# Kernel tuning notes

Hardware: AMD Instinct MI355X
Metric: run time of the kernel (lower is better)

## Reference

```python
import jax, jax.numpy as jnp
from jax import lax
import numpy as np

B = 4096        # num_batch
NVAR = 120      # 3 * num_legs(4) * horizon(10)
NC = 2 * NVAR   # num_constraints = 240
HID = 1024      # GRU hidden size
RIN = 3 * (NC + NVAR)  # GRU input dim = 1080
MAXITER = 8
RHO = 1.0
REG = 1e-4


def setup_inputs() -> dict:
    key = jax.random.key(0)
    ks = jax.random.split(key, 10)
    # SPD quadratic cost H, linear cost g, inequality constraints C x <= c
    M = jax.random.normal(ks[0], (NVAR, NVAR), jnp.float32)
    H = M @ M.T / NVAR + jnp.eye(NVAR, dtype=jnp.float32)
    g = jax.random.normal(ks[1], (NVAR,), jnp.float32)
    C = 0.1 * jax.random.normal(ks[2], (NC, NVAR), jnp.float32)
    c = jax.random.uniform(ks[3], (NC,), jnp.float32, 0.1, 1.0)
    lamda_init = jax.random.normal(ks[4], (B, NVAR), jnp.float32)
    s_init = jax.random.uniform(ks[5], (B, NC), jnp.float32)
    h_0 = jnp.zeros((B, HID), jnp.float32)
    # GRU cell (torch GRUCell layout: [3*HID, in]) + output head to NC+NVAR
    sc_i = 1.0 / np.sqrt(RIN)
    sc_h = 1.0 / np.sqrt(HID)
    W_ih = sc_i * jax.random.normal(ks[6], (3 * HID, RIN), jnp.float32)
    b_ih = jnp.zeros((3 * HID,), jnp.float32)
    W_hh = sc_h * jax.random.normal(ks[7], (3 * HID, HID), jnp.float32)
    b_hh = jnp.zeros((3 * HID,), jnp.float32)
    W_out = sc_h * jax.random.normal(ks[8], (NC + NVAR, HID), jnp.float32)
    b_out = jnp.zeros((NC + NVAR,), jnp.float32)
    return dict(lamda_init=lamda_init, s_init=s_init, h_0=h_0, H=H, g=g, C=C, c=c,
                W_ih=W_ih, b_ih=b_ih, W_hh=W_hh, b_hh=b_hh, W_out=W_out, b_out=b_out)


def _gru_cell(x, h, W_ih, b_ih, W_hh, b_hh):
    gi = x @ W_ih.T + b_ih
    gh = h @ W_hh.T + b_hh
    i_r, i_z, i_n = jnp.split(gi, 3, axis=1)
    h_r, h_z, h_n = jnp.split(gh, 3, axis=1)
    r = jax.nn.sigmoid(i_r + h_r)
    z = jax.nn.sigmoid(i_z + h_z)
    n = jnp.tanh(i_n + r * h_n)
    return (1.0 - z) * n + z * h


def reference(lamda_init, s_init, h_0, H, g, C, c, W_ih, b_ih, W_hh, b_hh, W_out, b_out):
    I = jnp.eye(NVAR, dtype=H.dtype)
    # ---- init solve (compute_projection_gru preamble) ----
    Q_inv0 = jnp.linalg.pinv(H + REG * I)
    lincost0 = -0.0 * lamda_init + g                 # [B, NVAR]
    xi0 = (-lincost0) @ Q_inv0.T                     # sol = (Qinv @ rhs.T).T
    s0 = jnp.maximum(0.0, -(xi0 @ C.T) + c)
    s0 = 0.0 * s_init + s0                           # s_init = 0*nn + 1*s_
    lam0 = lamda_init
    # ---- constant per-iteration projection matrix (same every iter) ----
    Q_inv = jnp.linalg.pinv(H + RHO * (C.T @ C) + REG * I)

    def step(carry, _):
        s, lam, h = carry
        # compute_feasible_control
        b_aug = c - s                                # [B, NC]
        lincost = -lam + g - RHO * (b_aug @ C)       # [B, NVAR]
        xi = (-lincost) @ Q_inv.T                    # [B, NVAR]
        Axi = xi @ C.T                               # [B, NC]
        s_new = jnp.maximum(0.0, -Axi + c)
        res_vec = Axi - c + s_new
        res_norm = jnp.linalg.norm(res_vec, axis=1)
        lam_new = lam - RHO * (res_vec @ C)
        qp_cost = 0.5 * (xi @ H @ xi.T) + xi @ g     # [B, B] (faithful to source)
        qp_norm = jnp.linalg.norm(qp_cost, axis=1)
        # GRU refinement
        r = jnp.concatenate([s, lam, s_new, lam_new, s_new - s, lam_new - lam], axis=1)
        h_new = _gru_cell(r, h, W_ih, b_ih, W_hh, b_hh)
        out = h_new @ W_out.T + b_out                # [B, NC+NVAR]
        s_fin = jnp.maximum(0.0, s_new + out[:, :NC])
        lam_fin = lam_new + out[:, NC:NC + NVAR]
        fixed = jnp.linalg.norm(lam - lam_fin, axis=1) + jnp.linalg.norm(s - s_fin, axis=1)
        return (s_fin, lam_fin, h_new), (xi, res_norm, fixed, qp_norm)

    (_, _, _), (xis, primal, fixed, qpres) = lax.scan(step, (s0, lam0, h_0), None, length=MAXITER)
    return xis[-1], primal, fixed, qpres
```

## Files before the change

### kernel.cpp

```cpp
#include <hip/hip_runtime.h>
#include <hip/hip_bf16.h>
#include <math.h>

#define NB    4096
#define NV    120
#define NCN   240
#define HIDD  1024
#define RINN  1080
#define NOUTD 360
#define NOUTP 384
#define NITER 8
#define REGEPS 1e-4f
#define NPART 128

#define KCAT 4224
#define HOFF 2176
#define KWC  2112
#define KWO  1024
#define NSTEP_R 34
#define NSTEPS  66

typedef unsigned short u16;
typedef __attribute__((ext_vector_type(8))) short short8v;
typedef __attribute__((ext_vector_type(4))) float f32x4;

__device__ inline u16 f2b(float x) {
    __hip_bfloat16 h = __float2bfloat16(x);
    return __builtin_bit_cast(u16, h);
}
__device__ inline float b2f(u16 u) {
    __hip_bfloat16 h = __builtin_bit_cast(__hip_bfloat16, u);
    return __bfloat162float(h);
}

__device__ inline void gl16(const void* g, void* l) {
    __builtin_amdgcn_global_load_lds(
        (__attribute__((address_space(1))) void*)(void*)g,
        (__attribute__((address_space(3))) void*)l, 16, 0, 0);
}

__global__ void k_buildA(const float* __restrict__ H, const float* __restrict__ C,
                         float* __restrict__ A, float* __restrict__ A0) {
    int i = blockIdx.x;
    int which = blockIdx.y;
    for (int j = threadIdx.x; j < NV; j += blockDim.x) {
        float v = H[i*NV + j] + (i == j ? REGEPS : 0.f);
        if (which == 0) {
            float acc = 0.f;
            for (int k = 0; k < NCN; ++k) acc += C[k*NV + i] * C[k*NV + j];
            A[i*NV + j] = v + acc;
        } else {
            A0[i*NV + j] = v;
        }
    }
}

__device__ inline void inv4x4(const float* m, float* inv) {
    float s0 = m[0]*m[5] - m[1]*m[4];
    float s1 = m[0]*m[6] - m[2]*m[4];
    float s2 = m[0]*m[7] - m[3]*m[4];
    float s3 = m[1]*m[6] - m[2]*m[5];
    float s4 = m[1]*m[7] - m[3]*m[5];
    float s5 = m[2]*m[7] - m[3]*m[6];
    float c5 = m[10]*m[15] - m[11]*m[14];
    float c4 = m[9]*m[15] - m[11]*m[13];
    float c3 = m[9]*m[14] - m[10]*m[13];
    float c2 = m[8]*m[15] - m[11]*m[12];
    float c1 = m[8]*m[14] - m[10]*m[12];
    float c0 = m[8]*m[13] - m[9]*m[12];
    float det = s0*c5 - s1*c4 + s2*c3 + s3*c2 - s4*c1 + s5*c0;
    float id = 1.0f / det;
    inv[0]  = ( m[5]*c5 - m[6]*c4 + m[7]*c3) * id;
    inv[1]  = (-m[1]*c5 + m[2]*c4 - m[3]*c3) * id;
    inv[2]  = ( m[13]*s5 - m[14]*s4 + m[15]*s3) * id;
    inv[3]  = (-m[9]*s5 + m[10]*s4 - m[11]*s3) * id;
    inv[4]  = (-m[4]*c5 + m[6]*c2 - m[7]*c1) * id;
    inv[5]  = ( m[0]*c5 - m[2]*c2 + m[3]*c1) * id;
    inv[6]  = (-m[12]*s5 + m[14]*s2 - m[15]*s1) * id;
    inv[7]  = ( m[8]*s5 - m[10]*s2 + m[11]*s1) * id;
    inv[8]  = ( m[4]*c4 - m[5]*c2 + m[7]*c0) * id;
    inv[9]  = (-m[0]*c4 + m[1]*c2 - m[3]*c0) * id;
    inv[10] = ( m[12]*s4 - m[13]*s2 + m[15]*s0) * id;
    inv[11] = (-m[8]*s4 + m[9]*s2 - m[11]*s0) * id;
    inv[12] = (-m[4]*c3 + m[5]*c1 - m[6]*c0) * id;
    inv[13] = ( m[0]*c3 - m[1]*c1 + m[2]*c0) * id;
    inv[14] = (-m[12]*s3 + m[13]*s1 - m[14]*s0) * id;
    inv[15] = ( m[8]*s3 - m[9]*s1 + m[10]*s0) * id;
}

__global__ __launch_bounds__(1024) void k_invert(const float* __restrict__ Ain,
                                                 const float* __restrict__ A0in,
                                                 float* __restrict__ Qi,
                                                 float* __restrict__ Qi0) {
    __shared__ float M[NV][132];
    __shared__ float Rl[4][132];
    __shared__ float Bl[16];
    const float* src = (blockIdx.x == 0) ? Ain : A0in;
    float* dst = (blockIdx.x == 0) ? Qi : Qi0;
    const int t = threadIdx.x;
    for (int idx = t; idx < NV*132; idx += 1024) {
        int i = idx / 132, j = idx - i*132;
        M[i][j] = (j < NV) ? src[i*NV + j] : 0.f;
    }
    __syncthreads();
    const int ty = t >> 5;
    const int g4 = (t & 31) * 4;
    for (int kk = 0; kk < NV; kk += 4) {
        if (ty == 0) {
            float a[16], b[16];
            #pragma unroll
            for (int p = 0; p < 4; ++p) {
                float4 v = *(const float4*)&M[kk + p][kk];
                a[p*4+0] = v.x; a[p*4+1] = v.y; a[p*4+2] = v.z; a[p*4+3] = v.w;
            }
            inv4x4(a, b);
            float4 m0v = *(const float4*)&M[kk+0][g4];
            float4 m1v = *(const float4*)&M[kk+1][g4];
            float4 m2v = *(const float4*)&M[kk+2][g4];
            float4 m3v = *(const float4*)&M[kk+3][g4];
            #pragma unroll
            for (int p = 0; p < 4; ++p) {
                float4 r;
                r.x = b[p*4+0]*m0v.x + b[p*4+1]*m1v.x + b[p*4+2]*m2v.x + b[p*4+3]*m3v.x;
                r.y = b[p*4+0]*m0v.y + b[p*4+1]*m1v.y + b[p*4+2]*m2v.y + b[p*4+3]*m3v.y;
                r.z = b[p*4+0]*m0v.z + b[p*4+1]*m1v.z + b[p*4+2]*m2v.z + b[p*4+3]*m3v.z;
                r.w = b[p*4+0]*m0v.w + b[p*4+1]*m1v.w + b[p*4+2]*m2v.w + b[p*4+3]*m3v.w;
                *(float4*)&Rl[p][g4] = r;
            }
            if (t < 16) Bl[t] = b[t];
        }
        float4 F[4];
        #pragma unroll
        for (int q = 0; q < 4; ++q) {
            int i = ty + 32*q;
            F[q] = (i < NV) ? *(const float4*)&M[i][kk] : float4{0.f,0.f,0.f,0.f};
        }
        __syncthreads();
        #pragma unroll
        for (int q = 0; q < 4; ++q) {
            int i = ty + 32*q;
            if (i < NV) {
                int dp = i - kk;
                bool ispiv = (dp >= 0) && (dp < 4);
                float4 v;
                if (g4 == kk) {
                    if (ispiv) {
                        v = *(const float4*)&Bl[dp*4];
                    } else {
                        v.x = -(F[q].x*Bl[0] + F[q].y*Bl[4] + F[q].z*Bl[8]  + F[q].w*Bl[12]);
                        v.y = -(F[q].x*Bl[1] + F[q].y*Bl[5] + F[q].z*Bl[9]  + F[q].w*Bl[13]);
                        v.z = -(F[q].x*Bl[2] + F[q].y*Bl[6] + F[q].z*Bl[10] + F[q].w*Bl[14]);
                        v.w = -(F[q].x*Bl[3] + F[q].y*Bl[7] + F[q].z*Bl[11] + F[q].w*Bl[15]);
                    }
                } else if (ispiv) {
                    v = *(const float4*)&Rl[dp][g4];
                } else {
                    float4 r0 = *(const float4*)&Rl[0][g4];
                    float4 r1 = *(const float4*)&Rl[1][g4];
                    float4 r2 = *(const float4*)&Rl[2][g4];
                    float4 r3 = *(const float4*)&Rl[3][g4];
                    v = *(const float4*)&M[i][g4];
                    v.x -= F[q].x*r0.x + F[q].y*r1.x + F[q].z*r2.x + F[q].w*r3.x;
                    v.y -= F[q].x*r0.y + F[q].y*r1.y + F[q].z*r2.y + F[q].w*r3.y;
                    v.z -= F[q].x*r0.z + F[q].y*r1.z + F[q].z*r2.z + F[q].w*r3.z;
                    v.w -= F[q].x*r0.w + F[q].y*r1.w + F[q].z*r2.w + F[q].w*r3.w;
                }
                *(float4*)&M[i][g4] = v;
            }
        }
        __syncthreads();
    }
    for (int idx = t; idx < NV*NV; idx += 1024) {
        int i = idx / NV, j = idx - i*NV;
        dst[idx] = M[i][j];
    }
}

__global__ void k_s0(const float* __restrict__ Qi0, const float* __restrict__ g,
                     const float* __restrict__ C, const float* __restrict__ c,
                     float* __restrict__ s0v) {
    __shared__ float xi0[NV];
    int t = threadIdx.x;
    if (t < NV) {
        float a = 0.f;
        for (int j = 0; j < NV; ++j) a += Qi0[t*NV + j] * g[j];
        xi0[t] = -a;
    }
    __syncthreads();
    if (t < NCN) {
        float a = 0.f;
        for (int j = 0; j < NV; ++j) a += C[t*NV + j] * xi0[j];
        s0v[t] = fmaxf(0.f, c[t] - a);
    }
}

__global__ void k_init(const float* __restrict__ s0v, const float* __restrict__ lam0,
                       float* __restrict__ s, float* __restrict__ lam) {
    int b0 = blockIdx.x * 8;
    int t = threadIdx.x;
    for (int idx = t; idx < 8*NCN; idx += 256) {
        int m = idx / NCN, k = idx % NCN;
        s[(size_t)(b0 + m)*NCN + k] = s0v[k];
    }
    for (int idx = t; idx < 8*NV; idx += 256) lam[(size_t)b0*NV + idx] = lam0[(size_t)b0*NV + idx];
}

__global__ void k_packH(const float* __restrict__ h0, u16* __restrict__ act) {
    int n = blockIdx.x;
    size_t base = (size_t)n * KCAT + HOFF;
    for (int k = threadIdx.x; k < HIDD; k += 256) {
        float x = h0[(size_t)n * HIDD + k];
        u16 hi = f2b(x);
        act[base + k] = hi;
        act[base + HIDD + k] = f2b(x - b2f(hi));
    }
}

__global__ void k_packWcat(const float* __restrict__ Wih, const float* __restrict__ Whh,
                           u16* __restrict__ Wc) {
    int n = blockIdx.x;
    size_t base = (size_t)n * KWC;
    for (int k = threadIdx.x; k < 1088; k += 256)
        Wc[base + k] = f2b(k < RINN ? Wih[(size_t)n * RINN + k] : 0.f);
    for (int k = threadIdx.x; k < HIDD; k += 256)
        Wc[base + 1088 + k] = f2b(Whh[(size_t)n * HIDD + k]);
}

__global__ void k_packWo(const float* __restrict__ src, u16* __restrict__ dst) {
    int n = blockIdx.x;
    size_t row = (size_t)n * KWO;
    for (int k = threadIdx.x; k < KWO; k += 256)
        dst[row + k] = f2b(n < NOUTD ? src[(size_t)n * HIDD + k] : 0.f);
}

__device__ inline void write2(u16* __restrict__ act, size_t base, int pos, float x) {
    u16 hi = f2b(x);
    u16 lo = f2b(x - b2f(hi));
    act[base + pos] = hi;
    act[base + 1088 + pos] = lo;
}

#define XB 8
__global__ __launch_bounds__(512) void k_xiproj(
        const float* __restrict__ s, const float* __restrict__ lam,
        const float* __restrict__ Cg, const float* __restrict__ c,
        const float* __restrict__ g, const float* __restrict__ Qi,
        const float* __restrict__ Hg,
        float* __restrict__ xi, float* __restrict__ Y, float* __restrict__ wv,
        float* __restrict__ snew, float* __restrict__ lamn,
        u16* __restrict__ act, float* __restrict__ primal) {
    __shared__ float Msh[NCN][125];
    __shared__ float bd[XB][NCN];
    __shared__ float ul[XB][NV];
    __shared__ float xl[XB][NV];
    __shared__ float resl[XB][NCN];
    const int b0 = blockIdx.x * XB;
    const int t = threadIdx.x;

    for (int idx = t; idx < XB*NCN; idx += 512) {
        int m = idx / NCN, k = idx % NCN;
        bd[m][k] = c[k] - s[(size_t)(b0 + m)*NCN + k];
    }
    for (int idx = t; idx < NCN*NV; idx += 512) {
        int i = idx / NV, j = idx - i*NV;
        Msh[i][j] = Cg[idx];
    }
    __syncthreads();
    for (int idx = t; idx < XB*NV; idx += 512) {
        int m = idx / NV, j = idx - m*NV;
        float a0 = 0.f, a1 = 0.f, a2 = 0.f, a3 = 0.f;
        for (int k = 0; k < NCN; k += 4) {
            a0 += bd[m][k]     * Msh[k][j];
            a1 += bd[m][k + 1] * Msh[k + 1][j];
            a2 += bd[m][k + 2] * Msh[k + 2][j];
            a3 += bd[m][k + 3] * Msh[k + 3][j];
        }
        ul[m][j] = lam[(size_t)(b0 + m)*NV + j] - g[j] + ((a0 + a1) + (a2 + a3));
    }
    __syncthreads();
    for (int idx = t; idx < NV*NV; idx += 512) {
        int i = idx / NV, j = idx - i*NV;
        Msh[i][j] = Qi[idx];
        Msh[120 + i][j] = Hg[idx];
    }
    __syncthreads();
    for (int idx = t; idx < XB*NV; idx += 512) {
        int m = idx / NV, i = idx - m*NV;
        float a0 = 0.f, a1 = 0.f, a2 = 0.f, a3 = 0.f;
        for (int j = 0; j < NV; j += 4) {
            a0 += Msh[j][i]     * ul[m][j];
            a1 += Msh[j + 1][i] * ul[m][j + 1];
            a2 += Msh[j + 2][i] * ul[m][j + 2];
            a3 += Msh[j + 3][i] * ul[m][j + 3];
        }
        float a = (a0 + a1) + (a2 + a3);
        xl[m][i] = a;
        xi[(size_t)(b0 + m)*NV + i] = a;
    }
    __syncthreads();
    for (int idx = t; idx < XB*NV; idx += 512) {
        int m = idx / NV, i = idx - m*NV;
        float a0 = 0.f, a1 = 0.f, a2 = 0.f, a3 = 0.f;
        for (int j = 0; j < NV; j += 4) {
            a0 += xl[m][j]     * Msh[120 + j][i];
            a1 += xl[m][j + 1] * Msh[121 + j][i];
            a2 += xl[m][j + 2] * Msh[122 + j][i];
            a3 += xl[m][j + 3] * Msh[123 + j][i];
        }
        Y[(size_t)(b0 + m)*NV + i] = (a0 + a1) + (a2 + a3);
    }
    if (t < XB) {
        float a = 0.f;
        for (int j = 0; j < NV; ++j) a += xl[t][j] * g[j];
        wv[b0 + t] = a;
    }
    __syncthreads();
    for (int idx = t; idx < NCN*NV; idx += 512) {
        int i = idx / NV, j = idx - i*NV;
        Msh[i][j] = Cg[idx];
    }
    __syncthreads();
    for (int idx = t; idx < XB*NCN; idx += 512) {
        int m = idx / NCN, k = idx - m*NCN;
        float a0 = 0.f, a1 = 0.f, a2 = 0.f, a3 = 0.f;
        for (int j = 0; j < NV; j += 4) {
            a0 += Msh[k][j]     * xl[m][j];
            a1 += Msh[k][j + 1] * xl[m][j + 1];
            a2 += Msh[k][j + 2] * xl[m][j + 2];
            a3 += Msh[k][j + 3] * xl[m][j + 3];
        }
        float a = (a0 + a1) + (a2 + a3);
        float sn = fmaxf(0.f, c[k] - a);
        float rv = a - c[k] + sn;
        resl[m][k] = rv;
        int b = b0 + m;
        snew[(size_t)b*NCN + k] = sn;
        float so = s[(size_t)b*NCN + k];
        size_t base = (size_t)b * KCAT;
        write2(act, base, k, so);
        write2(act, base, 360 + k, sn);
        write2(act, base, 720 + k, sn - so);
    }
    __syncthreads();
    if (t < XB) {
        float a = 0.f;
        for (int k = 0; k < NCN; ++k) a += resl[t][k] * resl[t][k];
        primal[b0 + t] = sqrtf(a);
    }
    for (int idx = t; idx < XB*NV; idx += 512) {
        int m = idx / NV, i = idx - m*NV;
        float a0 = 0.f, a1 = 0.f, a2 = 0.f, a3 = 0.f;
        for (int k = 0; k < NCN; k += 4) {
            a0 += resl[m][k]     * Msh[k][i];
            a1 += resl[m][k + 1] * Msh[k + 1][i];
            a2 += resl[m][k + 2] * Msh[k + 2][i];
            a3 += resl[m][k + 3] * Msh[k + 3][i];
        }
        float a = (a0 + a1) + (a2 + a3);
        int b = b0 + m;
        float lo = lam[(size_t)b*NV + i];
        float ln = lo - a;
        lamn[(size_t)b*NV + i] = ln;
        size_t base = (size_t)b * KCAT;
        write2(act, base, 240 + i, lo);
        write2(act, base, 600 + i, ln);
        write2(act, base, 960 + i, ln - lo);
    }
    for (int idx = t; idx < XB*8; idx += 512) {
        int m = idx >> 3, k = 1080 + (idx & 7);
        size_t base = (size_t)(b0 + m) * KCAT;
        act[base + k] = 0;
        act[base + 1088 + k] = 0;
    }
}

__global__ __launch_bounds__(256) void k_qp_part(const float* __restrict__ xi, const float* __restrict__ wv,
                         double* __restrict__ Gp, double* __restrict__ vp, double* __restrict__ Sp) {
    __shared__ float xl[32][NV];
    __shared__ float wl[32];
    int p = blockIdx.x;
    int b0 = p * 32;
    int t = threadIdx.x;
    for (int idx = t; idx < 32*NV; idx += 256) xl[idx/NV][idx%NV] = xi[(size_t)b0*NV + idx];
    if (t < 32) wl[t] = wv[b0 + t];
    __syncthreads();
    for (int idx = t; idx < NV*NV; idx += 256) {
        int i = idx / NV, j = idx % NV;
        double a = 0.0;
        for (int m = 0; m < 32; ++m) a += (double)xl[m][i] * (double)xl[m][j];
        Gp[(size_t)p*NV*NV + idx] = a;
    }
    if (t < NV) {
        double a = 0.0;
        for (int m = 0; m < 32; ++m) a += (double)wl[m] * (double)xl[m][t];
        vp[(size_t)p*NV + t] = a;
    }
    if (t == 0) {
        double a = 0.0;
        for (int m = 0; m < 32; ++m) a += (double)wl[m] * (double)wl[m];
        Sp[p] = a;
    }
}

__global__ void k_qp_red(const double* __restrict__ Gp, const double* __restrict__ vp,
                         const double* __restrict__ Sp,
                         double* __restrict__ G, double* __restrict__ v, double* __restrict__ S) {
    int idx = blockIdx.x * 256 + threadIdx.x;
    if (idx < NV*NV) {
        double a = 0.0;
        for (int p = 0; p < NPART; ++p) a += Gp[(size_t)p*NV*NV + idx];
        G[idx] = a;
    }
    if (idx < NV) {
        double a = 0.0;
        for (int p = 0; p < NPART; ++p) a += vp[(size_t)p*NV + idx];
        v[idx] = a;
    }
    if (idx == 0) {
        double a = 0.0;
        for (int p = 0; p < NPART; ++p) a += Sp[p];
        S[0] = a;
    }
}

__global__ __launch_bounds__(256) void k_qp_norm(const float* __restrict__ Y, const double* __restrict__ G,
                         const double* __restrict__ v, const double* __restrict__ S,
                         float* __restrict__ qp) {
    __shared__ float Yl[16][NV];
    __shared__ double tl[16][NV];
    int b0 = blockIdx.x * 16;
    int t = threadIdx.x;
    for (int idx = t; idx < 16*NV; idx += 256) Yl[idx/NV][idx%NV] = Y[(size_t)b0*NV + idx];
    __syncthreads();
    for (int idx = t; idx < 16*NV; idx += 256) {
        int m = idx / NV, i = idx % NV;
        double a = 0.0;
        for (int j = 0; j < NV; ++j) a += G[j*NV + i] * (double)Yl[m][j];
        tl[m][i] = a;
    }
    __syncthreads();
    if (t < 16) {
        double a = 0.0, bv = 0.0;
        for (int i = 0; i < NV; ++i) { a += (double)Yl[t][i] * tl[t][i]; bv += (double)Yl[t][i] * v[i]; }
        double q = 0.25 * a + bv + S[0];
        qp[b0 + t] = (float)sqrt(q > 0.0 ? q : 0.0);
    }
}

#define GRUF_STEP(NSLOT, BUFI) do {                                              \
    char* Ah_ = lds + (BUFI) * 40960;                                            \
    char* Al_ = Ah_ + 8192;                                                      \
    char* Bb_ = Ah_ + 16384;                                                     \
    const int srow = lane & 15;                                                  \
    const int ksl = lane >> 4;                                                   \
    short8v ah[2], al[2];                                                        \
    _Pragma("unroll")                                                            \
    for (int fm = 0; fm < 2; ++fm) {                                             \
        int rr = wm * 32 + fm * 16 + srow;                                       \
        int off = rr * 64 + ((ksl ^ ((rr >> 1) & 3)) << 4);                      \
        ah[fm] = *(const short8v*)(Ah_ + off);                                   \
        al[fm] = *(const short8v*)(Al_ + off);                                   \
    }                                                                            \
    __builtin_amdgcn_s_setprio(1);                                               \
    _Pragma("unroll")                                                            \
    for (int fn = 0; fn < 2; ++fn) {                                             \
        int rb = wn * 32 + fn * 16 + srow;                                       \
        int boff = rb * 64 + ((ksl ^ ((rb >> 1) & 3)) << 4);                     \
        short8v bfr = *(const short8v*)(Bb_ + boff);                             \
        short8v bfz = *(const short8v*)(Bb_ + 8192 + boff);                      \
        short8v bfn = *(const short8v*)(Bb_ + 16384 + boff);                     \
        _Pragma("unroll")                                                        \
        for (int fm = 0; fm < 2; ++fm) {                                         \
            acc[0][fn][fm] = __builtin_amdgcn_mfma_f32_16x16x32_bf16(ah[fm], bfr, acc[0][fn][fm], 0, 0, 0); \
            acc[0][fn][fm] = __builtin_amdgcn_mfma_f32_16x16x32_bf16(al[fm], bfr, acc[0][fn][fm], 0, 0, 0); \
            acc[1][fn][fm] = __builtin_amdgcn_mfma_f32_16x16x32_bf16(ah[fm], bfz, acc[1][fn][fm], 0, 0, 0); \
            acc[1][fn][fm] = __builtin_amdgcn_mfma_f32_16x16x32_bf16(al[fm], bfz, acc[1][fn][fm], 0, 0, 0); \
            acc[NSLOT][fn][fm] = __builtin_amdgcn_mfma_f32_16x16x32_bf16(ah[fm], bfn, acc[NSLOT][fn][fm], 0, 0, 0); \
            acc[NSLOT][fn][fm] = __builtin_amdgcn_mfma_f32_16x16x32_bf16(al[fm], bfn, acc[NSLOT][fn][fm], 0, 0, 0); \
        }                                                                        \
    }                                                                            \
    __builtin_amdgcn_s_setprio(0);                                               \
} while (0)

#define GRUF_SYNCN do {                                                          \
    if (wid < 8) { asm volatile("s_waitcnt vmcnt(3)" ::: "memory"); }            \
    else         { asm volatile("s_waitcnt vmcnt(2)" ::: "memory"); }            \
    __builtin_amdgcn_s_barrier();                                                \
    __builtin_amdgcn_sched_barrier(0);                                           \
} while (0)
#define GRUF_SYNC0 do {                                                          \
    asm volatile("s_waitcnt vmcnt(0)" ::: "memory");                             \
    __builtin_amdgcn_s_barrier();                                                \
    __builtin_amdgcn_sched_barrier(0);                                           \
} while (0)

__global__ __launch_bounds__(1024) void k_gruf(
        const u16* __restrict__ act,
        const u16* __restrict__ Wc,
        const float* __restrict__ bih, const float* __restrict__ bhh,
        u16* __restrict__ actn) {
    __shared__ char lds[122880];
    const int t = threadIdx.x;
    const int lane = t & 63;
    const int wid = t >> 6;
    const int wm = wid >> 2;
    const int wn = wid & 3;
    const int bid = blockIdx.x;
    const int xcd = bid & 7;
    const int slot = bid >> 3;
    const int m0 = (xcd * 4 + (slot & 3)) * 128;
    const int n0 = (slot >> 2) * 128;

    f32x4 acc[4][2][2];
    #pragma unroll
    for (int i = 0; i < 4; ++i)
        #pragma unroll
        for (int j = 0; j < 2; ++j)
            #pragma unroll
            for (int k = 0; k < 2; ++k) {
                f32x4 z = {0.f, 0.f, 0.f, 0.f};
                acc[i][j][k] = z;
            }

    auto stage = [&](int step) {
        char* Ah_ = lds + (step % 3) * 40960;
        char* Al_ = Ah_ + 8192;
        char* Bb_ = Ah_ + 16384;
        const int hiOff = (step < NSTEP_R) ? step * 32 : step * 32 + 1088;
        const int loOff = hiOff + ((step < NSTEP_R) ? 1088 : 1024);
        const int wOff = step * 32;
        if (wid >= 8) {
            int q = wid - 8;
            int rr = q * 16 + (lane >> 2);
            int kq = ((lane & 3) ^ ((rr >> 1) & 3)) << 3;
            gl16(act + (size_t)(m0 + rr) * KCAT + hiOff + kq, Ah_ + q * 1024);
            gl16(act + (size_t)(m0 + rr) * KCAT + loOff + kq, Al_ + q * 1024);
        } else {
            #pragma unroll
            for (int j = 0; j < 3; ++j) {
                int cb = wid * 3 + j;
                int rbg = cb * 16 + (lane >> 2);
                int kq = ((lane & 3) ^ ((rbg >> 1) & 3)) << 3;
                gl16(Wc + (size_t)((rbg >> 7) * 1024 + n0 + (rbg & 127)) * KWC + wOff + kq,
                     Bb_ + cb * 1024);
            }
        }
    };

    stage(0);
    stage(1);
    GRUF_SYNCN;
    for (int step = 0; step < NSTEP_R; ++step) {
        stage(step + 2);
        GRUF_STEP(2, step % 3);
        GRUF_SYNCN;
    }
    for (int step = NSTEP_R; step < NSTEPS; ++step) {
        if (step + 2 < NSTEPS) {
            stage(step + 2);
            GRUF_STEP(3, step % 3);
            GRUF_SYNCN;
        } else {
            GRUF_STEP(3, step % 3);
            GRUF_SYNC0;
        }
    }

    #pragma unroll
    for (int fn = 0; fn < 2; ++fn) {
        const int jj = n0 + wn * 32 + fn * 16 + (lane & 15);
        const float bir = bih[jj],        bhr = bhh[jj];
        const float biz = bih[1024 + jj], bhz = bhh[1024 + jj];
        const float bin = bih[2048 + jj], bhn = bhh[2048 + jj];
        #pragma unroll
        for (int fm = 0; fm < 2; ++fm) {
            #pragma unroll
            for (int rg = 0; rg < 4; ++rg) {
                int m = m0 + wm * 32 + fm * 16 + (lane >> 4) * 4 + rg;
                float rz = acc[0][fn][fm][rg];
                float zz = acc[1][fn][fm][rg];
                float inn = acc[2][fn][fm][rg];
                float hnn = acc[3][fn][fm][rg];
                float rgate = 1.f / (1.f + expf(-(rz + bir + bhr)));
                float zgate = 1.f / (1.f + expf(-(zz + biz + bhz)));
                float ngate = tanhf(inn + bin + rgate * (hnn + bhn));
                size_t base = (size_t)m * KCAT + HOFF;
                float hv = b2f(act[base + jj]) + b2f(act[base + HIDD + jj]);
                float hnew = (1.f - zgate) * ngate + zgate * hv;
                u16 nh = f2b(hnew);
                actn[base + jj] = nh;
                actn[base + HIDD + jj] = f2b(hnew - b2f(nh));
            }
        }
    }
}

__global__ __launch_bounds__(512, 2) void k_outp(
        const u16* __restrict__ act, const u16* __restrict__ Wo,
        const float* __restrict__ bo, float* __restrict__ outb) {
    __shared__ char lds[49152];
    const int t = threadIdx.x;
    const int lane = t & 63;
    const int wid = t >> 6;
    const int wm = wid >> 2;
    const int wn = wid & 3;
    const int m0 = blockIdx.x * 128;
    const int n0 = blockIdx.y * 128;
    f32x4 acc[2][4];
    #pragma unroll
    for (int i = 0; i < 2; ++i)
        #pragma unroll
        for (int j = 0; j < 4; ++j) {
            f32x4 z = {0.f, 0.f, 0.f, 0.f};
            acc[i][j] = z;
        }

    auto stage = [&](int step, int buf) {
        char* Ah_ = lds + buf * 24576;
        char* Al_ = Ah_ + 8192;
        char* Bb_ = Ah_ + 16384;
        const int hiOff = HOFF + step * 32;
        const int loOff = HOFF + HIDD + step * 32;
        int s = (wid << 6) + lane;
        int rr = s >> 2;
        int kq = ((lane & 3) ^ ((rr >> 1) & 3)) << 3;
        gl16(act + (size_t)(m0 + rr) * KCAT + hiOff + kq, Ah_ + wid * 1024);
        gl16(act + (size_t)(m0 + rr) * KCAT + loOff + kq, Al_ + wid * 1024);
        gl16(Wo + (size_t)(n0 + rr) * KWO + step * 32 + kq, Bb_ + wid * 1024);
    };

    stage(0, 0);
    __syncthreads();
    int cur = 0;
    for (int step = 0; step < 32; ++step) {
        if (step + 1 < 32) stage(step + 1, cur ^ 1);
        {
            char* Ah_ = lds + cur * 24576;
            char* Al_ = Ah_ + 8192;
            char* Bb_ = Ah_ + 16384;
            const int srow = lane & 15;
            const int ksl = lane >> 4;
            short8v ah[4], al[4];
            #pragma unroll
            for (int fm = 0; fm < 4; ++fm) {
                int rr = wm * 64 + fm * 16 + srow;
                int off = rr * 64 + ((ksl ^ ((rr >> 1) & 3)) << 4);
                ah[fm] = *(const short8v*)(Ah_ + off);
                al[fm] = *(const short8v*)(Al_ + off);
            }
            #pragma unroll
            for (int fn = 0; fn < 2; ++fn) {
                int rb = wn * 32 + fn * 16 + srow;
                int boff = rb * 64 + ((ksl ^ ((rb >> 1) & 3)) << 4);
                short8v bf = *(const short8v*)(Bb_ + boff);
                #pragma unroll
                for (int fm = 0; fm < 4; ++fm) {
                    acc[fn][fm] = __builtin_amdgcn_mfma_f32_16x16x32_bf16(ah[fm], bf, acc[fn][fm], 0, 0, 0);
                    acc[fn][fm] = __builtin_amdgcn_mfma_f32_16x16x32_bf16(al[fm], bf, acc[fn][fm], 0, 0, 0);
                }
            }
        }
        __syncthreads();
        cur ^= 1;
    }
    #pragma unroll
    for (int fn = 0; fn < 2; ++fn) {
        int n = n0 + wn * 32 + fn * 16 + (lane & 15);
        if (n < NOUTD) {
            float bb = bo[n];
            #pragma unroll
            for (int fm = 0; fm < 4; ++fm) {
                #pragma unroll
                for (int rg = 0; rg < 4; ++rg) {
                    int m = m0 + wm * 64 + fm * 16 + (lane >> 4) * 4 + rg;
                    outb[(size_t)m * NOUTP + n] = acc[fn][fm][rg] + bb;
                }
            }
        }
    }
}

__global__ __launch_bounds__(256) void k_fin(const float* __restrict__ snew, const float* __restrict__ lamn,
                     const float* __restrict__ outb,
                     float* __restrict__ s, float* __restrict__ lam,
                     float* __restrict__ fx) {
    __shared__ float redS[16][17];
    __shared__ float redL[16][17];
    int b0 = blockIdx.x * 16;
    int tm = threadIdx.x / 16;
    int tk = threadIdx.x % 16;
    int b = b0 + tm;
    float ds2 = 0.f, dl2 = 0.f;
    for (int k = tk; k < NCN; k += 16) {
        float o = outb[(size_t)b*NOUTP + k];
        float sf = fmaxf(0.f, snew[(size_t)b*NCN + k] + o);
        float so = s[(size_t)b*NCN + k];
        s[(size_t)b*NCN + k] = sf;
        float d = so - sf;
        ds2 += d * d;
    }
    for (int i = tk; i < NV; i += 16) {
        float o = outb[(size_t)b*NOUTP + NCN + i];
        float lf = lamn[(size_t)b*NV + i] + o;
        float lo = lam[(size_t)b*NV + i];
        lam[(size_t)b*NV + i] = lf;
        float d = lo - lf;
        dl2 += d * d;
    }
    redS[tm][tk] = ds2;
    redL[tm][tk] = dl2;
    __syncthreads();
    if (tk == 0) {
        float a = 0.f, l = 0.f;
        for (int q = 0; q < 16; ++q) { a += redS[tm][q]; l += redL[tm][q]; }
        fx[b] = sqrtf(l) + sqrtf(a);
    }
}

extern "C" void kernel_launch(void* const* d_in, const int* in_sizes, int n_in,
                              void* d_out, int out_size, void* d_ws, size_t ws_size,
                              hipStream_t stream) {
    const float* lamda_init = (const float*)d_in[0];
    const float* h0    = (const float*)d_in[2];
    const float* H     = (const float*)d_in[3];
    const float* g     = (const float*)d_in[4];
    const float* C     = (const float*)d_in[5];
    const float* c     = (const float*)d_in[6];
    const float* W_ih  = (const float*)d_in[7];
    const float* b_ih  = (const float*)d_in[8];
    const float* W_hh  = (const float*)d_in[9];
    const float* b_hh  = (const float*)d_in[10];
    const float* W_out = (const float*)d_in[11];
    const float* b_out = (const float*)d_in[12];

    float* out    = (float*)d_out;
    float* xi_out = out;
    float* primal = out + (size_t)NB*NV;
    float* fixedo = primal + (size_t)NITER*NB;
    float* qpres  = fixedo + (size_t)NITER*NB;

    char* wp = (char*)d_ws;
    auto alloc = [&](size_t bytes) {
        void* p = (void*)wp;
        wp += (bytes + 255) & ~(size_t)255;
        return p;
    };
    float* Amat  = (float*)alloc(NV*NV*4);
    float* A0m   = (float*)alloc(NV*NV*4);
    float* Qinv  = (float*)alloc(NV*NV*4);
    float* Qinv0 = (float*)alloc(NV*NV*4);
    float* s0v   = (float*)alloc(NCN*4);
    float* sbuf  = (float*)alloc((size_t)NB*NCN*4);
    float* snew  = (float*)alloc((size_t)NB*NCN*4);
    float* lam   = (float*)alloc((size_t)NB*NV*4);
    float* lamn  = (float*)alloc((size_t)NB*NV*4);
    float* xib   = (float*)alloc((size_t)NB*NV*4);
    float* Yb    = (float*)alloc((size_t)NB*NV*4);
    float* wb    = (float*)alloc(NB*4);
    float* outb  = (float*)alloc((size_t)NB*NOUTP*4);
    u16* actA    = (u16*)alloc((size_t)NB*KCAT*2);
    u16* actB    = (u16*)alloc((size_t)NB*KCAT*2);
    u16* Wcat    = (u16*)alloc((size_t)3072*KWC*2);
    u16* Wopk    = (u16*)alloc((size_t)NOUTP*KWO*2);
    double* Gpart = (double*)alloc((size_t)NPART*NV*NV*8);
    double* vpart = (double*)alloc((size_t)NPART*NV*8);
    double* Spart = (double*)alloc(NPART*8);
    double* Gfin  = (double*)alloc(NV*NV*8);
    double* vfin  = (double*)alloc(NV*8);
    double* Sfin  = (double*)alloc(8);

    k_buildA<<<dim3(NV, 2), dim3(128), 0, stream>>>(H, C, Amat, A0m);
    k_invert<<<dim3(2), dim3(1024), 0, stream>>>(Amat, A0m, Qinv, Qinv0);
    k_s0<<<dim3(1), dim3(256), 0, stream>>>(Qinv0, g, C, c, s0v);
    k_init<<<dim3(NB/8), dim3(256), 0, stream>>>(s0v, lamda_init, sbuf, lam);
    k_packWcat<<<dim3(3072), dim3(256), 0, stream>>>(W_ih, W_hh, Wcat);
    k_packWo<<<dim3(NOUTP), dim3(256), 0, stream>>>(W_out, Wopk);
    k_packH<<<dim3(NB), dim3(256), 0, stream>>>(h0, actA);

    u16* hc = actA;
    u16* hn2 = actB;
    for (int it = 0; it < NITER; ++it) {
        k_xiproj<<<dim3(NB/XB), dim3(512), 0, stream>>>(sbuf, lam, C, c, g, Qinv, H,
                                                        xib, Yb, wb, snew, lamn, hc,
                                                        primal + (size_t)it*NB);
        k_qp_part<<<dim3(NPART), dim3(256), 0, stream>>>(xib, wb, Gpart, vpart, Spart);
        k_qp_red<<<dim3((NV*NV + 255)/256), dim3(256), 0, stream>>>(Gpart, vpart, Spart, Gfin, vfin, Sfin);
        k_qp_norm<<<dim3(NB/16), dim3(256), 0, stream>>>(Yb, Gfin, vfin, Sfin, qpres + (size_t)it*NB);
        k_gruf<<<dim3(256), dim3(1024), 0, stream>>>(hc, Wcat, b_ih, b_hh, hn2);
        k_outp<<<dim3(NB/128, 3), dim3(512), 0, stream>>>(hn2, Wopk, b_out, outb);
        k_fin<<<dim3(NB/16), dim3(256), 0, stream>>>(snew, lamn, outb, sbuf, lam, fixedo + (size_t)it*NB);
        u16* tmp = hc; hc = hn2; hn2 = tmp;
    }
    hipMemcpyAsync(xi_out, xib, (size_t)NB*NV*sizeof(float), hipMemcpyDeviceToDevice, stream);
}
```

Measured before the change: 2.438 ms.

## Shrink GRU and output GEMM tiles, use double buffering, and split QP partials finer

The fused GRU GEMM drops from 128x128 tiles on 1024-thread blocks with a three-stage asynchronous pipeline to 64x128 tiles on 512-thread blocks with plain double buffering and __syncthreads. The setprio hints and the fine-grained vmcnt waits are removed. The output projection moves to 64-row tiles, which doubles its grid, and the QP Gram partials use 16 rows per block across 256 partitions. The goal is more blocks for occupancy and load balance across CUs, at the cost of less weight reuse per tile, more global traffic, and a shallower prefetch pipeline.

```diff
diff --git a/kernel.cpp b/kernel.cpp
--- a/kernel.cpp
+++ b/kernel.cpp
@@ -11,7 +11,7 @@
 #define NOUTP 384
 #define NITER 8
 #define REGEPS 1e-4f
-#define NPART 128
+#define NPART 256
 
 #define KCAT 4224
 #define HOFF 2176
@@ -376,28 +376,28 @@
 
 __global__ __launch_bounds__(256) void k_qp_part(const float* __restrict__ xi, const float* __restrict__ wv,
                          double* __restrict__ Gp, double* __restrict__ vp, double* __restrict__ Sp) {
-    __shared__ float xl[32][NV];
-    __shared__ float wl[32];
+    __shared__ float xl[16][NV];
+    __shared__ float wl[16];
     int p = blockIdx.x;
-    int b0 = p * 32;
+    int b0 = p * 16;
     int t = threadIdx.x;
-    for (int idx = t; idx < 32*NV; idx += 256) xl[idx/NV][idx%NV] = xi[(size_t)b0*NV + idx];
-    if (t < 32) wl[t] = wv[b0 + t];
+    for (int idx = t; idx < 16*NV; idx += 256) xl[idx/NV][idx%NV] = xi[(size_t)b0*NV + idx];
+    if (t < 16) wl[t] = wv[b0 + t];
     __syncthreads();
     for (int idx = t; idx < NV*NV; idx += 256) {
         int i = idx / NV, j = idx % NV;
         double a = 0.0;
-        for (int m = 0; m < 32; ++m) a += (double)xl[m][i] * (double)xl[m][j];
+        for (int m = 0; m < 16; ++m) a += (double)xl[m][i] * (double)xl[m][j];
         Gp[(size_t)p*NV*NV + idx] = a;
     }
     if (t < NV) {
         double a = 0.0;
-        for (int m = 0; m < 32; ++m) a += (double)wl[m] * (double)xl[m][t];
+        for (int m = 0; m < 16; ++m) a += (double)wl[m] * (double)xl[m][t];
         vp[(size_t)p*NV + t] = a;
     }
     if (t == 0) {
         double a = 0.0;
-        for (int m = 0; m < 32; ++m) a += (double)wl[m] * (double)wl[m];
+        for (int m = 0; m < 16; ++m) a += (double)wl[m] * (double)wl[m];
         Sp[p] = a;
     }
 }
@@ -448,9 +448,9 @@
 }
 
 #define GRUF_STEP(NSLOT, BUFI) do {                                              \
-    char* Ah_ = lds + (BUFI) * 40960;                                            \
-    char* Al_ = Ah_ + 8192;                                                      \
-    char* Bb_ = Ah_ + 16384;                                                     \
+    char* Ah_ = lds + (BUFI) * 32768;                                            \
+    char* Al_ = Ah_ + 4096;                                                      \
+    char* Bb_ = Ah_ + 8192;                                                      \
     const int srow = lane & 15;                                                  \
     const int ksl = lane >> 4;                                                   \
     short8v ah[2], al[2];                                                        \
@@ -461,7 +461,6 @@
         ah[fm] = *(const short8v*)(Ah_ + off);                                   \
         al[fm] = *(const short8v*)(Al_ + off);                                   \
     }                                                                            \
-    __builtin_amdgcn_s_setprio(1);                                               \
     _Pragma("unroll")                                                            \
     for (int fn = 0; fn < 2; ++fn) {                                             \
         int rb = wn * 32 + fn * 16 + srow;                                       \
@@ -479,27 +478,14 @@
             acc[NSLOT][fn][fm] = __builtin_amdgcn_mfma_f32_16x16x32_bf16(al[fm], bfn, acc[NSLOT][fn][fm], 0, 0, 0); \
         }                                                                        \
     }                                                                            \
-    __builtin_amdgcn_s_setprio(0);                                               \
 } while (0)
 
-#define GRUF_SYNCN do {                                                          \
-    if (wid < 8) { asm volatile("s_waitcnt vmcnt(3)" ::: "memory"); }            \
-    else         { asm volatile("s_waitcnt vmcnt(2)" ::: "memory"); }            \
-    __builtin_amdgcn_s_barrier();                                                \
-    __builtin_amdgcn_sched_barrier(0);                                           \
-} while (0)
-#define GRUF_SYNC0 do {                                                          \
-    asm volatile("s_waitcnt vmcnt(0)" ::: "memory");                             \
-    __builtin_amdgcn_s_barrier();                                                \
-    __builtin_amdgcn_sched_barrier(0);                                           \
-} while (0)
-
-__global__ __launch_bounds__(1024) void k_gruf(
+__global__ __launch_bounds__(512) void k_gruf(
         const u16* __restrict__ act,
         const u16* __restrict__ Wc,
         const float* __restrict__ bih, const float* __restrict__ bhh,
         u16* __restrict__ actn) {
-    __shared__ char lds[122880];
+    __shared__ char lds[65536];
     const int t = threadIdx.x;
     const int lane = t & 63;
     const int wid = t >> 6;
@@ -508,8 +494,8 @@
     const int bid = blockIdx.x;
     const int xcd = bid & 7;
     const int slot = bid >> 3;
-    const int m0 = (xcd * 4 + (slot & 3)) * 128;
-    const int n0 = (slot >> 2) * 128;
+    const int m0 = (xcd * 8 + (slot & 7)) * 64;
+    const int n0 = (slot >> 3) * 128;
 
     f32x4 acc[4][2][2];
     #pragma unroll
@@ -522,48 +508,45 @@
                 acc[i][j][k] = z;
             }
 
-    auto stage = [&](int step) {
-        char* Ah_ = lds + (step % 3) * 40960;
-        char* Al_ = Ah_ + 8192;
-        char* Bb_ = Ah_ + 16384;
+    auto stage = [&](int step, int buf) {
+        char* Ah_ = lds + buf * 32768;
+        char* Al_ = Ah_ + 4096;
+        char* Bb_ = Ah_ + 8192;
         const int hiOff = (step < NSTEP_R) ? step * 32 : step * 32 + 1088;
         const int loOff = hiOff + ((step < NSTEP_R) ? 1088 : 1024);
         const int wOff = step * 32;
-        if (wid >= 8) {
-            int q = wid - 8;
-            int rr = q * 16 + (lane >> 2);
+        {
+            int rr = (wid & 3) * 16 + (lane >> 2);
             int kq = ((lane & 3) ^ ((rr >> 1) & 3)) << 3;
-            gl16(act + (size_t)(m0 + rr) * KCAT + hiOff + kq, Ah_ + q * 1024);
-            gl16(act + (size_t)(m0 + rr) * KCAT + loOff + kq, Al_ + q * 1024);
-        } else {
-            #pragma unroll
-            for (int j = 0; j < 3; ++j) {
-                int cb = wid * 3 + j;
-                int rbg = cb * 16 + (lane >> 2);
-                int kq = ((lane & 3) ^ ((rbg >> 1) & 3)) << 3;
-                gl16(Wc + (size_t)((rbg >> 7) * 1024 + n0 + (rbg & 127)) * KWC + wOff + kq,
-                     Bb_ + cb * 1024);
-            }
+            if (wid < 4)
+                gl16(act + (size_t)(m0 + rr) * KCAT + hiOff + kq, Ah_ + (wid & 3) * 1024);
+            else
+                gl16(act + (size_t)(m0 + rr) * KCAT + loOff + kq, Al_ + (wid & 3) * 1024);
+        }
+        #pragma unroll
+        for (int j = 0; j < 3; ++j) {
+            int cb = wid * 3 + j;
+            int rbg = cb * 16 + (lane >> 2);
+            int kq = ((lane & 3) ^ ((rbg >> 1) & 3)) << 3;
+            gl16(Wc + (size_t)((rbg >> 7) * 1024 + n0 + (rbg & 127)) * KWC + wOff + kq,
+                 Bb_ + cb * 1024);
         }
     };
 
-    stage(0);
-    stage(1);
-    GRUF_SYNCN;
+    stage(0, 0);
+    __syncthreads();
+    int cur = 0;
     for (int step = 0; step < NSTEP_R; ++step) {
-        stage(step + 2);
-        GRUF_STEP(2, step % 3);
-        GRUF_SYNCN;
+        stage(step + 1, cur ^ 1);
+        GRUF_STEP(2, cur);
+        __syncthreads();
+        cur ^= 1;
     }
     for (int step = NSTEP_R; step < NSTEPS; ++step) {
-        if (step + 2 < NSTEPS) {
-            stage(step + 2);
-            GRUF_STEP(3, step % 3);
-            GRUF_SYNCN;
-        } else {
-            GRUF_STEP(3, step % 3);
-            GRUF_SYNC0;
-        }
+        if (step + 1 < NSTEPS) stage(step + 1, cur ^ 1);
+        GRUF_STEP(3, cur);
+        __syncthreads();
+        cur ^= 1;
     }
 
     #pragma unroll
@@ -595,38 +578,45 @@
     }
 }
 
-__global__ __launch_bounds__(512, 2) void k_outp(
+__global__ __launch_bounds__(512) void k_outp(
         const u16* __restrict__ act, const u16* __restrict__ Wo,
         const float* __restrict__ bo, float* __restrict__ outb) {
-    __shared__ char lds[49152];
+    __shared__ char lds[32768];
     const int t = threadIdx.x;
     const int lane = t & 63;
     const int wid = t >> 6;
     const int wm = wid >> 2;
     const int wn = wid & 3;
-    const int m0 = blockIdx.x * 128;
+    const int m0 = blockIdx.x * 64;
     const int n0 = blockIdx.y * 128;
-    f32x4 acc[2][4];
+    f32x4 acc[2][2];
     #pragma unroll
     for (int i = 0; i < 2; ++i)
         #pragma unroll
-        for (int j = 0; j < 4; ++j) {
+        for (int j = 0; j < 2; ++j) {
             f32x4 z = {0.f, 0.f, 0.f, 0.f};
             acc[i][j] = z;
         }
 
     auto stage = [&](int step, int buf) {
-        char* Ah_ = lds + buf * 24576;
-        char* Al_ = Ah_ + 8192;
-        char* Bb_ = Ah_ + 16384;
-        const int hiOff = HOFF + step * 32;
-        const int loOff = HOFF + HIDD + step * 32;
-        int s = (wid << 6) + lane;
-        int rr = s >> 2;
-        int kq = ((lane & 3) ^ ((rr >> 1) & 3)) << 3;
-        gl16(act + (size_t)(m0 + rr) * KCAT + hiOff + kq, Ah_ + wid * 1024);
-        gl16(act + (size_t)(m0 + rr) * KCAT + loOff + kq, Al_ + wid * 1024);
-        gl16(Wo + (size_t)(n0 + rr) * KWO + step * 32 + kq, Bb_ + wid * 1024);
+        char* Ah_ = lds + buf * 16384;
+        char* Al_ = Ah_ + 4096;
+        char* Bb_ = Ah_ + 8192;
+        {
+            int rr = (wid & 3) * 16 + (lane >> 2);
+            int kq = ((lane & 3) ^ ((rr >> 1) & 3)) << 3;
+            if (wid < 4)
+                gl16(act + (size_t)(m0 + rr) * KCAT + HOFF + step * 32 + kq,
+                     Ah_ + (wid & 3) * 1024);
+            else
+                gl16(act + (size_t)(m0 + rr) * KCAT + HOFF + HIDD + step * 32 + kq,
+                     Al_ + (wid & 3) * 1024);
+        }
+        {
+            int rb = wid * 16 + (lane >> 2);
+            int kq = ((lane & 3) ^ ((rb >> 1) & 3)) << 3;
+            gl16(Wo + (size_t)(n0 + rb) * KWO + step * 32 + kq, Bb_ + wid * 1024);
+        }
     };
 
     stage(0, 0);
@@ -635,15 +625,15 @@
     for (int step = 0; step < 32; ++step) {
         if (step + 1 < 32) stage(step + 1, cur ^ 1);
         {
-            char* Ah_ = lds + cur * 24576;
-            char* Al_ = Ah_ + 8192;
-            char* Bb_ = Ah_ + 16384;
+            char* Ah_ = lds + cur * 16384;
+            char* Al_ = Ah_ + 4096;
+            char* Bb_ = Ah_ + 8192;
             const int srow = lane & 15;
             const int ksl = lane >> 4;
-            short8v ah[4], al[4];
+            short8v ah[2], al[2];
             #pragma unroll
-            for (int fm = 0; fm < 4; ++fm) {
-                int rr = wm * 64 + fm * 16 + srow;
+            for (int fm = 0; fm < 2; ++fm) {
+                int rr = wm * 32 + fm * 16 + srow;
                 int off = rr * 64 + ((ksl ^ ((rr >> 1) & 3)) << 4);
                 ah[fm] = *(const short8v*)(Ah_ + off);
                 al[fm] = *(const short8v*)(Al_ + off);
@@ -654,7 +644,7 @@
                 int boff = rb * 64 + ((ksl ^ ((rb >> 1) & 3)) << 4);
                 short8v bf = *(const short8v*)(Bb_ + boff);
                 #pragma unroll
-                for (int fm = 0; fm < 4; ++fm) {
+                for (int fm = 0; fm < 2; ++fm) {
                     acc[fn][fm] = __builtin_amdgcn_mfma_f32_16x16x32_bf16(ah[fm], bf, acc[fn][fm], 0, 0, 0);
                     acc[fn][fm] = __builtin_amdgcn_mfma_f32_16x16x32_bf16(al[fm], bf, acc[fn][fm], 0, 0, 0);
                 }
@@ -669,10 +659,10 @@
         if (n < NOUTD) {
             float bb = bo[n];
             #pragma unroll
-            for (int fm = 0; fm < 4; ++fm) {
+            for (int fm = 0; fm < 2; ++fm) {
                 #pragma unroll
                 for (int rg = 0; rg < 4; ++rg) {
-                    int m = m0 + wm * 64 + fm * 16 + (lane >> 4) * 4 + rg;
+                    int m = m0 + wm * 32 + fm * 16 + (lane >> 4) * 4 + rg;
                     outb[(size_t)m * NOUTP + n] = acc[fn][fm][rg] + bb;
                 }
             }
@@ -786,8 +776,8 @@
         k_qp_part<<<dim3(NPART), dim3(256), 0, stream>>>(xib, wb, Gpart, vpart, Spart);
         k_qp_red<<<dim3((NV*NV + 255)/256), dim3(256), 0, stream>>>(Gpart, vpart, Spart, Gfin, vfin, Sfin);
         k_qp_norm<<<dim3(NB/16), dim3(256), 0, stream>>>(Yb, Gfin, vfin, Sfin, qpres + (size_t)it*NB);
-        k_gruf<<<dim3(256), dim3(1024), 0, stream>>>(hc, Wcat, b_ih, b_hh, hn2);
-        k_outp<<<dim3(NB/128, 3), dim3(512), 0, stream>>>(hn2, Wopk, b_out, outb);
+        k_gruf<<<dim3(512), dim3(512), 0, stream>>>(hc, Wcat, b_ih, b_hh, hn2);
+        k_outp<<<dim3(64, 3), dim3(512), 0, stream>>>(hn2, Wopk, b_out, outb);
         k_fin<<<dim3(NB/16), dim3(256), 0, stream>>>(snew, lamn, outb, sbuf, lam, fixedo + (size_t)it*NB);
         u16* tmp = hc; hc = hn2; hn2 = tmp;
     }
```

Result: faster. 2.356 ms (-3.3%).
